# Performance work log

Measured on AMD Instinct MI355X. Metric: run time of the kernel, lower is better.

## Reference

```python
import jax, jax.numpy as jnp
import numpy as np

B, T, I, H, O = 64, 256, 128, 512, 64
GRAD_CLIP = 5.0


def setup_inputs() -> dict:
    key = jax.random.key(0)
    ks = jax.random.split(key, 20)
    sH = 1.0 / np.sqrt(H)
    sI = 1.0 / np.sqrt(I)
    f32 = jnp.float32
    return {
        "x": jax.random.normal(ks[0], (B, T, I), f32),
        "y": jax.random.randint(ks[1], (B,), 0, O),
        "W1w": jax.random.normal(ks[2], (H, H), f32) * sH,
        "V1w": jax.random.normal(ks[3], (H, I), f32) * sI,
        "V1b": jnp.zeros((H,), f32),
        "W2w": jax.random.normal(ks[4], (H, H), f32) * sH,
        "W2b": jnp.zeros((H,), f32),
        "V2w": jax.random.normal(ks[5], (H, I), f32) * sI,
        "W3w": jax.random.normal(ks[6], (H, H), f32) * sH,
        "W3b": jnp.zeros((H,), f32),
        "V3w": jax.random.normal(ks[7], (H, I), f32) * sI,
        "Woutw": jax.random.normal(ks[8], (O, H), f32) * sH,
        "Woutb": jnp.zeros((O,), f32),
        "BW1": jax.random.normal(ks[9], (O, H), f32) * sH,
        "BV1": jax.random.normal(ks[10], (O, H), f32) * sH,
        "BW2": jax.random.normal(ks[11], (O, H), f32) * sH,
        "BV2": jax.random.normal(ks[12], (O, H), f32) * sH,
        "BW3": jax.random.normal(ks[13], (O, H), f32) * sH,
        "BV3": jax.random.normal(ks[14], (O, H), f32) * sH,
    }


def reference(x, y, W1w, V1w, V1b, W2w, W2b, V2w, W3w, W3b, V3w,
              Woutw, Woutb, BW1, BV1, BW2, BV2, BW3, BV3):
    Bsz, Tlen, _ = x.shape
    Hd = W1w.shape[0]
    Od = Woutw.shape[0]
    h0 = jnp.zeros((Bsz, Hd), x.dtype)
    xt = jnp.swapaxes(x, 0, 1)  # [T, B, I]

    def step(h, xti):
        z = jax.nn.sigmoid(h @ W2w.T + W2b + xti @ V2w.T)
        r = jax.nn.sigmoid(h @ W3w.T + W3b + xti @ V3w.T)
        ht = jnp.tanh(xti @ V1w.T + V1b + (h * r) @ W1w.T)
        hn = (1.0 - z) * ht + z * h
        return hn, (r, z, ht, hn)

    hT, (rs, zs, hs, hid) = jax.lax.scan(step, h0, xt)  # each [T, B, H]
    output = jax.nn.softmax(hT @ Woutw.T + Woutb, axis=-1)
    error = output - jax.nn.one_hot(y, Od, dtype=output.dtype)

    BW1e, BV1e = error @ BW1, error @ BV1
    BW2e, BV2e = error @ BW2, error @ BV2
    BW3e, BV3e = error @ BW3, error @ BV3

    hiddens = jnp.concatenate([h0[None], hid], axis=0)  # [T+1, B, H]
    # Faithfully replicate torch's hiddens[t-1] list indexing: at t=0 this is
    # hiddens[-1], i.e. the FINAL hidden state (Python negative indexing).
    idx = (np.arange(Tlen) - 1) % (Tlen + 1)
    hprev = hiddens[idx]  # [T, B, H]

    rr = rs * (1.0 - rs)
    sz = 1.0 - zs
    dh = 1.0 - hs ** 2

    # z-gate terms (index 1) -- original code uses r*(1-r) here, replicated.
    zg = (hprev - hs) * rr
    zgV = zg * BV2e[None]
    zgW = zg * BW2e[None]
    dV1 = jnp.einsum('tbh,tbi->hi', zgV, xt) / Bsz
    dW1 = jnp.einsum('tbh,tbH->hH', zgW, hprev) / Bsz
    db1 = zgV.sum(0).mean(0)

    # r-gate terms (index 2)
    AV = ((BV3e[None] * sz * dh) @ W1w.T) * hprev * rr
    AW = ((BW3e[None] * sz * dh) @ W1w.T) * hprev * rr
    dV2 = jnp.einsum('tbh,tbi->hi', AV, xt) / Bsz
    dW2 = jnp.einsum('tbh,tbH->hH', AW, hprev) / Bsz
    db2 = AV.sum(0).mean(0)

    # h-gate terms (index 0)
    HV = ((BV1e[None] * sz) @ W1w.T) * dh
    HW = ((BW1e[None] * sz) @ W1w.T) * dh
    dV0 = jnp.einsum('tbh,tbi->hi', HV, xt) / Bsz
    dW0 = jnp.einsum('tbh,tbH->hH', HW, rs * hprev) / Bsz
    db0 = HV.sum(0).mean(0)

    def nc(g):
        g = g / jnp.linalg.norm(g)
        return jnp.clip(g, -GRAD_CLIP, GRAD_CLIP)

    return (output, hT,
            nc(dW0), nc(dW1), nc(dW2),
            nc(dV0), nc(dV1), nc(dV2),
            nc(db0), nc(db1), nc(db2),
            error)
```

## Files before the change

### kernel.cpp

```cpp
#include <hip/hip_runtime.h>
#include <hip/hip_bf16.h>

#define DI __device__ __forceinline__

typedef __bf16 bf16x8 __attribute__((ext_vector_type(8)));
typedef __bf16 bf16x4 __attribute__((ext_vector_type(4)));
typedef __bf16 bf16x2 __attribute__((ext_vector_type(2)));
typedef float  f32x4  __attribute__((ext_vector_type(4)));
typedef unsigned long long ull;

static constexpr int Bc = 64, Tc = 256, Ic = 128, Hc = 512, Oc = 64;
static constexpr int TBc = Tc * Bc;
static constexpr size_t THW = (size_t)TBc * Hc;

static constexpr size_t O_OUT = 0;
static constexpr size_t O_HT  = 4096;
static constexpr size_t O_DW0 = 36864;
static constexpr size_t O_DV0 = 823296;
static constexpr size_t O_DB0 = 1019904;
static constexpr size_t O_ERR = 1021440;

static constexpr size_t W_SLOT = 1024;
static constexpr size_t W_DB   = 2048;
static constexpr size_t W_FLG  = 8192;
static constexpr size_t W_ERRW = 16384;
static constexpr size_t W_PROJ = 32768;
static constexpr size_t W_W1B  = 819200;
static constexpr size_t W_HX   = 1343488;
static constexpr size_t W_HRX  = 1474560;
static constexpr size_t W_XT   = 1605632;
static constexpr size_t W_HIST = 5799936;
static constexpr size_t W_PB   = 72908800;
static constexpr size_t W_NEED = W_PB + 100663296;


DI void st32_agent(float* p, float v) {
  __hip_atomic_store((unsigned int*)p, __float_as_uint(v),
                     __ATOMIC_RELAXED, __HIP_MEMORY_SCOPE_AGENT);
}
DI ull ld64_agent(const void* p) {
  return __hip_atomic_load((ull*)p, __ATOMIC_RELAXED, __HIP_MEMORY_SCOPE_AGENT);
}

DI void group_barrier(int* flags_g, int myslot, int bar, bool& dead) {
  __syncthreads();
  if (threadIdx.x == 0)
    __hip_atomic_store(&flags_g[myslot * 32], bar,
                       __ATOMIC_RELAXED, __HIP_MEMORY_SCOPE_AGENT);
  if (threadIdx.x < 64 && !dead) {
    const int l = threadIdx.x;
    int spins = 0;
    for (;;) {
      int v = bar;
      if (l < 16)
        v = __hip_atomic_load(&flags_g[l * 32],
                              __ATOMIC_RELAXED, __HIP_MEMORY_SCOPE_AGENT);
      if (__all(v >= bar)) break;
      __builtin_amdgcn_s_sleep(1);
      if (++spins > 4000000) { dead = true; break; }
    }
  }
  __syncthreads();
}

DI float hprev_at(const __bf16* __restrict__ h_h, int k, int col) {
  int t = k >> 6;
  if (t == 1) return 0.f;
  int row = (t == 0) ? (16320 + (k & 63)) : (k - 128);
  return (float)h_h[(size_t)row * 512 + col];
}


__global__ void kzero(float* __restrict__ p, int n) {
  int i = blockIdx.x * 256 + threadIdx.x;
  if (i < n) p[i] = 0.f;
}
__global__ void ksent(float* p, float v) { p[0] = v; }
__global__ void k0_cast(const float* __restrict__ s, __bf16* __restrict__ d, int n) {
  int i = blockIdx.x * 256 + threadIdx.x;
  if (i < n) d[i] = (__bf16)s[i];
}

__global__ __launch_bounds__(256)
void k1_xv(const float* __restrict__ x, const float* __restrict__ V1w,
           const float* __restrict__ V2w, const float* __restrict__ V3w,
           const float* __restrict__ V1b, const float* __restrict__ W2b,
           const float* __restrict__ W3b,
           float* __restrict__ xv1f, float* __restrict__ xv2f, float* __restrict__ xv3f)
{
  const int cb = blockIdx.x, t = blockIdx.y;
  const int g = cb >> 3, jblk = cb & 7;
  const float* Vg   = (g == 0) ? V1w : (g == 1) ? V2w : V3w;
  const float* bias = (g == 0) ? V1b : (g == 1) ? W2b : W3b;
  float* of = (g == 0) ? xv1f : (g == 1) ? xv2f : xv3f;
  __shared__ float As[64 * 69];
  __shared__ float Bs[64 * 69];
  const int tid = threadIdx.x;
  float acc[4][4] = {};
  const int m0 = (tid & 15) * 4, j0 = (tid >> 4) * 4;
  for (int kc = 0; kc < 2; ++kc) {
    __syncthreads();
    #pragma unroll
    for (int e = 0; e < 4; ++e) {
      int idx = tid + e * 256;
      int row = idx >> 4, c4 = (idx & 15) * 4;
      float4 v = *reinterpret_cast<const float4*>(&x[((size_t)row * 256 + t) * 128 + kc * 64 + c4]);
      As[row * 69 + c4 + 0] = v.x; As[row * 69 + c4 + 1] = v.y;
      As[row * 69 + c4 + 2] = v.z; As[row * 69 + c4 + 3] = v.w;
      float4 w = *reinterpret_cast<const float4*>(&Vg[(size_t)(jblk * 64 + row) * 128 + kc * 64 + c4]);
      Bs[row * 69 + c4 + 0] = w.x; Bs[row * 69 + c4 + 1] = w.y;
      Bs[row * 69 + c4 + 2] = w.z; Bs[row * 69 + c4 + 3] = w.w;
    }
    __syncthreads();
    for (int i = 0; i < 64; ++i) {
      float a[4], b[4];
      #pragma unroll
      for (int u = 0; u < 4; ++u) a[u] = As[(m0 + u) * 69 + i];
      #pragma unroll
      for (int u = 0; u < 4; ++u) b[u] = Bs[(j0 + u) * 69 + i];
      #pragma unroll
      for (int mi = 0; mi < 4; ++mi)
        #pragma unroll
        for (int ji = 0; ji < 4; ++ji) acc[mi][ji] += a[mi] * b[ji];
    }
  }
  #pragma unroll
  for (int ji = 0; ji < 4; ++ji) {
    int jg = jblk * 64 + j0 + ji;
    float bv = bias[jg];
    #pragma unroll
    for (int mi = 0; mi < 4; ++mi) {
      int b = m0 + mi;
      of[((size_t)t * 64 + b) * 512 + jg] = acc[mi][ji] + bv;
    }
  }
}

__global__ void e0_xt(const float* __restrict__ x, __bf16* __restrict__ XT)
{
  const int t = blockIdx.x;
  __shared__ __bf16 xs[64 * 132];
  const int tid = threadIdx.x;
  #pragma unroll
  for (int e = 0; e < 8; ++e) {
    int idx = tid + e * 256;
    int b = idx >> 5, c4 = (idx & 31) * 4;
    float4 v = *reinterpret_cast<const float4*>(&x[((size_t)b * 256 + t) * 128 + c4]);
    xs[b * 132 + c4 + 0] = (__bf16)v.x; xs[b * 132 + c4 + 1] = (__bf16)v.y;
    xs[b * 132 + c4 + 2] = (__bf16)v.z; xs[b * 132 + c4 + 3] = (__bf16)v.w;
  }
  __syncthreads();
  #pragma unroll
  for (int e = 0; e < 8; ++e) {
    int idx = tid + e * 256;
    int i = idx >> 4, b4 = (idx & 15) * 4;
    __bf16* d = &XT[(size_t)i * TBc + t * 64 + b4];
    d[0] = xs[(b4 + 0) * 132 + i];
    d[1] = xs[(b4 + 1) * 132 + i];
    d[2] = xs[(b4 + 2) * 132 + i];
    d[3] = xs[(b4 + 3) * 132 + i];
  }
}

__global__ __launch_bounds__(256, 1)
void k2_recur(const float* __restrict__ W1w, const float* __restrict__ W2w,
              const float* __restrict__ W3w,
              const float* __restrict__ xv1, const float* __restrict__ xv2,
              const float* __restrict__ xv3,
              __bf16* __restrict__ r_h, __bf16* __restrict__ z_h,
              __bf16* __restrict__ ht_h, __bf16* __restrict__ h_h,
              float* __restrict__ hx, float* __restrict__ hrx,
              int* __restrict__ flags, float* __restrict__ dout)
{
  const int g  = blockIdx.x >> 4;
  const int cw = blockIdx.x & 15;
  const int tid = threadIdx.x, lane = tid & 63, wv = tid >> 6;
  const int kh = wv & 1;
  const int ct = wv >> 1;
  const int q  = lane >> 4;
  const int colc = cw * 32 + ct * 16 + (lane & 15);
  const bool owner = (kh == 0);

  __shared__ __align__(16) __bf16 c0[8192];
  __shared__ __align__(16) __bf16 c1[8192];
  __shared__ __align__(16) __bf16 c2[8192];
  __shared__ float pbuf[128 * 9];

  bf16x8 w1c[3][8], w2c[3][8], w3c[3][8];
  #pragma unroll
  for (int kk2 = 0; kk2 < 8; ++kk2) {
    const int kb = (kh * 8 + kk2) * 32 + q * 8;
    #pragma unroll
    for (int j = 0; j < 8; ++j) {
      float w = W1w[(size_t)colc * 512 + kb + j];
      __bf16 a = (__bf16)w; float r1 = w - (float)a;
      __bf16 b = (__bf16)r1;
      w1c[0][kk2][j] = a; w1c[1][kk2][j] = b; w1c[2][kk2][j] = (__bf16)(r1 - (float)b);
      w = W2w[(size_t)colc * 512 + kb + j];
      a = (__bf16)w; r1 = w - (float)a; b = (__bf16)r1;
      w2c[0][kk2][j] = a; w2c[1][kk2][j] = b; w2c[2][kk2][j] = (__bf16)(r1 - (float)b);
      w = W3w[(size_t)colc * 512 + kb + j];
      a = (__bf16)w; r1 = w - (float)a; b = (__bf16)r1;
      w3c[0][kk2][j] = a; w3c[1][kk2][j] = b; w3c[2][kk2][j] = (__bf16)(r1 - (float)b);
    }
  }
  for (int i = tid; i < 8192; i += 256) {
    c0[i] = (__bf16)0.f; c1[i] = (__bf16)0.f; c2[i] = (__bf16)0.f;
  }
  __syncthreads();

  float hreg[4] = {0.f, 0.f, 0.f, 0.f};
  float* hx_g  = hx  + g * 8192;
  float* hrx_g = hrx + g * 8192;
  int* flags_g = flags + g * 16 * 32;
  const int fragbase = (colc >> 5) * 512 + (((colc >> 3) & 3) * 16 + q * 4) * 8 + (colc & 7);
  const int pb = (ct * 64 + lane) * 9;

  auto stage = [&](const float* __restrict__ srcf) {
    const ull* src = reinterpret_cast<const ull*>(srcf);
    ull u[16];
    #pragma unroll
    for (int j = 0; j < 16; ++j) u[j] = ld64_agent(src + j * 256 + tid);
    #pragma unroll
    for (int j = 0; j < 16; ++j) {
      float f0 = __uint_as_float((unsigned int)u[j]);
      float f1 = __uint_as_float((unsigned int)(u[j] >> 32));
      __bf16 a0 = (__bf16)f0; float r0 = f0 - (float)a0; __bf16 b0 = (__bf16)r0;
      __bf16 d0 = (__bf16)(r0 - (float)b0);
      __bf16 a1 = (__bf16)f1; float r1 = f1 - (float)a1; __bf16 b1 = (__bf16)r1;
      __bf16 d1 = (__bf16)(r1 - (float)b1);
      int o = (j * 256 + tid) * 2;
      bf16x2 v0; v0[0] = a0; v0[1] = a1;
      bf16x2 v1; v1[0] = b0; v1[1] = b1;
      bf16x2 v2; v2[0] = d0; v2[1] = d1;
      *reinterpret_cast<bf16x2*>(&c0[o]) = v0;
      *reinterpret_cast<bf16x2*>(&c1[o]) = v1;
      *reinterpret_cast<bf16x2*>(&c2[o]) = v2;
    }
  };

  bool dead = false;
  int bar = 0;
  #pragma unroll 1
  for (int t = 0; t < Tc; ++t) {
    const size_t rowb = ((size_t)t * 64 + g * 16 + q * 4) * 512 + colc;
    float xv1v[4], xv2v[4], xv3v[4];
    if (owner) {
      #pragma unroll
      for (int i = 0; i < 4; ++i) {
        size_t o = rowb + (size_t)i * 512;
        xv1v[i] = xv1[o]; xv2v[i] = xv2[o]; xv3v[i] = xv3[o];
      }
    }
    f32x4 a2 = {0.f,0.f,0.f,0.f}, a3 = {0.f,0.f,0.f,0.f};
    #pragma unroll
    for (int kk2 = 0; kk2 < 8; ++kk2) {
      const int idx = (kh * 8 + kk2) * 512 + lane * 8;
      bf16x8 h0 = *reinterpret_cast<const bf16x8*>(&c0[idx]);
      bf16x8 h1 = *reinterpret_cast<const bf16x8*>(&c1[idx]);
      bf16x8 h2 = *reinterpret_cast<const bf16x8*>(&c2[idx]);
      a2 = __builtin_amdgcn_mfma_f32_16x16x32_bf16(h0, w2c[0][kk2], a2, 0, 0, 0);
      a2 = __builtin_amdgcn_mfma_f32_16x16x32_bf16(h1, w2c[0][kk2], a2, 0, 0, 0);
      a2 = __builtin_amdgcn_mfma_f32_16x16x32_bf16(h0, w2c[1][kk2], a2, 0, 0, 0);
      a2 = __builtin_amdgcn_mfma_f32_16x16x32_bf16(h2, w2c[0][kk2], a2, 0, 0, 0);
      a2 = __builtin_amdgcn_mfma_f32_16x16x32_bf16(h1, w2c[1][kk2], a2, 0, 0, 0);
      a2 = __builtin_amdgcn_mfma_f32_16x16x32_bf16(h0, w2c[2][kk2], a2, 0, 0, 0);
      a3 = __builtin_amdgcn_mfma_f32_16x16x32_bf16(h0, w3c[0][kk2], a3, 0, 0, 0);
      a3 = __builtin_amdgcn_mfma_f32_16x16x32_bf16(h1, w3c[0][kk2], a3, 0, 0, 0);
      a3 = __builtin_amdgcn_mfma_f32_16x16x32_bf16(h0, w3c[1][kk2], a3, 0, 0, 0);
      a3 = __builtin_amdgcn_mfma_f32_16x16x32_bf16(h2, w3c[0][kk2], a3, 0, 0, 0);
      a3 = __builtin_amdgcn_mfma_f32_16x16x32_bf16(h1, w3c[1][kk2], a3, 0, 0, 0);
      a3 = __builtin_amdgcn_mfma_f32_16x16x32_bf16(h0, w3c[2][kk2], a3, 0, 0, 0);
    }
    if (!owner) {
      #pragma unroll
      for (int i = 0; i < 4; ++i) { pbuf[pb + i] = a2[i]; pbuf[pb + 4 + i] = a3[i]; }
    }
    __syncthreads();
    float zz[4], rr4[4];
    if (owner) {
      #pragma unroll
      for (int i = 0; i < 4; ++i) {
        float s2 = a2[i] + pbuf[pb + i]     + xv2v[i];
        float s3 = a3[i] + pbuf[pb + 4 + i] + xv3v[i];
        zz[i]  = 1.f / (1.f + expf(-s2));
        rr4[i] = 1.f / (1.f + expf(-s3));
        st32_agent(&hrx_g[fragbase + i * 8], hreg[i] * rr4[i]);
      }
    }
    ++bar; group_barrier(flags_g, cw, bar, dead);
    if (owner) {
      #pragma unroll
      for (int i = 0; i < 4; ++i) {
        z_h[rowb + (size_t)i * 512] = (__bf16)zz[i];
        r_h[rowb + (size_t)i * 512] = (__bf16)rr4[i];
      }
    }
    stage(hrx_g);
    __syncthreads();
    f32x4 a1 = {0.f,0.f,0.f,0.f};
    #pragma unroll
    for (int kk2 = 0; kk2 < 8; ++kk2) {
      const int idx = (kh * 8 + kk2) * 512 + lane * 8;
      bf16x8 h0 = *reinterpret_cast<const bf16x8*>(&c0[idx]);
      bf16x8 h1 = *reinterpret_cast<const bf16x8*>(&c1[idx]);
      bf16x8 h2 = *reinterpret_cast<const bf16x8*>(&c2[idx]);
      a1 = __builtin_amdgcn_mfma_f32_16x16x32_bf16(h0, w1c[0][kk2], a1, 0, 0, 0);
      a1 = __builtin_amdgcn_mfma_f32_16x16x32_bf16(h1, w1c[0][kk2], a1, 0, 0, 0);
      a1 = __builtin_amdgcn_mfma_f32_16x16x32_bf16(h0, w1c[1][kk2], a1, 0, 0, 0);
      a1 = __builtin_amdgcn_mfma_f32_16x16x32_bf16(h2, w1c[0][kk2], a1, 0, 0, 0);
      a1 = __builtin_amdgcn_mfma_f32_16x16x32_bf16(h1, w1c[1][kk2], a1, 0, 0, 0);
      a1 = __builtin_amdgcn_mfma_f32_16x16x32_bf16(h0, w1c[2][kk2], a1, 0, 0, 0);
    }
    if (!owner) {
      #pragma unroll
      for (int i = 0; i < 4; ++i) pbuf[pb + i] = a1[i];
    }
    __syncthreads();
    float htv[4];
    if (owner) {
      #pragma unroll
      for (int i = 0; i < 4; ++i) {
        float pre = a1[i] + pbuf[pb + i] + xv1v[i];
        float ht = tanhf(pre);
        float hn = zz[i] * (hreg[i] - ht) + ht;
        htv[i] = ht;
        hreg[i] = hn;
        st32_agent(&hx_g[fragbase + i * 8], hn);
      }
    }
    ++bar; group_barrier(flags_g, cw, bar, dead);
    if (owner) {
      #pragma unroll
      for (int i = 0; i < 4; ++i) {
        ht_h[rowb + (size_t)i * 512] = (__bf16)htv[i];
        h_h[rowb + (size_t)i * 512]  = (__bf16)hreg[i];
      }
    }
    if (t + 1 < Tc) stage(hx_g);
    __syncthreads();
  }
  if (owner) {
    #pragma unroll
    for (int i = 0; i < 4; ++i) {
      int b = g * 16 + q * 4 + i;
      dout[O_HT + (size_t)b * 512 + colc] = hreg[i];
    }
  }
}

__global__ void k3a_soft(const float* __restrict__ Woutw, const float* __restrict__ Woutb,
                         const int* __restrict__ y, float* __restrict__ dout,
                         float* __restrict__ errw)
{
  const int b = blockIdx.x, o = threadIdx.x;
  const float* hrow = dout + O_HT + (size_t)b * 512;
  float sv = Woutb[o];
  for (int k = 0; k < 512; ++k) sv += hrow[k] * Woutw[(size_t)o * 512 + k];
  float mx = sv;
  for (int off = 32; off; off >>= 1) mx = fmaxf(mx, __shfl_xor(mx, off, 64));
  float e = expf(sv - mx);
  float sum = e;
  for (int off = 32; off; off >>= 1) sum += __shfl_xor(sum, off, 64);
  float outp = e / sum;
  float errv = outp - ((y[b] == o) ? 1.f : 0.f);
  dout[O_OUT + b * 64 + o] = outp;
  dout[O_ERR + b * 64 + o] = errv;
  errw[b * 64 + o] = errv;
}

__global__ __launch_bounds__(256)
void k3b_proj(const float* __restrict__ err,
              const float* b0, const float* b1, const float* b2,
              const float* b3, const float* b4, const float* b5,
              float* __restrict__ proj)
{
  const int p = blockIdx.y;
  const int hb = blockIdx.x * 64;
  const float* BX = (p==0)?b0:(p==1)?b1:(p==2)?b2:(p==3)?b3:(p==4)?b4:b5;
  __shared__ float es[64 * 64];
  __shared__ float bs[64 * 65];
  for (int i = threadIdx.x; i < 4096; i += 256) es[i] = err[i];
  for (int i = threadIdx.x; i < 4096; i += 256) {
    int o = i >> 6, hh = i & 63;
    bs[o * 65 + hh] = BX[(size_t)o * 512 + hb + hh];
  }
  __syncthreads();
  for (int e = 0; e < 16; ++e) {
    int idx = threadIdx.x + e * 256;
    int b = idx >> 6, hh = idx & 63;
    float s = 0.f;
    for (int o = 0; o < 64; ++o) s += es[b * 64 + o] * bs[o * 65 + hh];
    proj[(size_t)p * 32768 + b * 512 + hb + hh] = s;
  }
}

__global__ __launch_bounds__(256)
void e1t(const __bf16* __restrict__ r_h, const __bf16* __restrict__ h_h,
         __bf16* __restrict__ HpT, __bf16* __restrict__ RsHpT)
{
  const int t = blockIdx.y, hb = blockIdx.x * 64;
  const int tid = threadIdx.x;
  __shared__ __bf16 tr[64 * 68];
  float hpv[16], rv[16];
  #pragma unroll
  for (int e = 0; e < 16; ++e) {
    int idx = tid + e * 256;
    int b = idx >> 6, hl = idx & 63;
    hpv[e] = hprev_at(h_h, t * 64 + b, hb + hl);
    rv[e]  = (float)r_h[((size_t)t * 64 + b) * 512 + hb + hl];
  }
  for (int rnd = 0; rnd < 2; ++rnd) {
    __syncthreads();
    #pragma unroll
    for (int e = 0; e < 16; ++e) {
      int idx = tid + e * 256;
      int b = idx >> 6, hl = idx & 63;
      tr[b * 68 + hl] = (__bf16)(rnd == 0 ? hpv[e] : rv[e] * hpv[e]);
    }
    __syncthreads();
    __bf16* dst = (rnd == 0) ? HpT : RsHpT;
    #pragma unroll
    for (int e = 0; e < 16; ++e) {
      int idx = tid + e * 256;
      int hl2 = idx >> 6, b2 = idx & 63;
      dst[(size_t)(hb + hl2) * TBc + t * 64 + b2] = tr[b2 * 68 + hl2];
    }
  }
}

__global__ __launch_bounds__(256)
void k4_pgemm(const __bf16* __restrict__ z_h, const __bf16* __restrict__ ht_h,
              const __bf16* __restrict__ r_h, const __bf16* __restrict__ h_h,
              const float* __restrict__ proj, const __bf16* __restrict__ W1b,
              __bf16* __restrict__ P)
{
  const int p = blockIdx.z;
  const int krow0 = blockIdx.x * 128;
  const int n0 = blockIdx.y * 128;
  const int pidx = (p == 0) ? 5 : (p == 1) ? 4 : (p == 2) ? 1 : 0;
  const float* pr = proj + (size_t)pidx * 32768;
  const int tid = threadIdx.x, lane = tid & 63, wv = tid >> 6, q = lane >> 4;
  const int wm = (wv & 1) * 64, wn = (wv >> 1) * 64;
  __shared__ __align__(16) __bf16 Al[128 * 40];
  __shared__ __align__(16) __bf16 Bl[128 * 40];
  f32x4 acc[4][4] = {};
  for (int kt = 0; kt < 16; ++kt) {
    const int h0 = kt * 32;
    __syncthreads();
    #pragma unroll
    for (int e = 0; e < 4; ++e) {
      int idx = tid + e * 256;
      int row = idx >> 3, h4 = (idx & 7) * 4;
      int kg = krow0 + row;
      bf16x4 zz = *reinterpret_cast<const bf16x4*>(&z_h[(size_t)kg * 512 + h0 + h4]);
      bf16x4 tt = *reinterpret_cast<const bf16x4*>(&ht_h[(size_t)kg * 512 + h0 + h4]);
      float4 pv = *reinterpret_cast<const float4*>(&pr[(size_t)(kg & 63) * 512 + h0 + h4]);
      float pvv[4] = {pv.x, pv.y, pv.z, pv.w};
      bf16x4 gv;
      #pragma unroll
      for (int j = 0; j < 4; ++j) {
        float sz = 1.f - (float)zz[j];
        float v = pvv[j] * sz;
        if (p < 2) { float h = (float)tt[j]; v *= (1.f - h * h); }
        gv[j] = (__bf16)v;
      }
      *reinterpret_cast<bf16x4*>(&Al[row * 40 + h4]) = gv;
      bf16x4 wv4 = *reinterpret_cast<const bf16x4*>(&W1b[(size_t)(n0 + row) * 512 + h0 + h4]);
      *reinterpret_cast<bf16x4*>(&Bl[row * 40 + h4]) = wv4;
    }
    __syncthreads();
    bf16x8 af[4], bfv[4];
    #pragma unroll
    for (int mi = 0; mi < 4; ++mi)
      af[mi] = *reinterpret_cast<const bf16x8*>(&Al[(wm + mi * 16 + (lane & 15)) * 40 + q * 8]);
    #pragma unroll
    for (int ni = 0; ni < 4; ++ni)
      bfv[ni] = *reinterpret_cast<const bf16x8*>(&Bl[(wn + ni * 16 + (lane & 15)) * 40 + q * 8]);
    #pragma unroll
    for (int mi = 0; mi < 4; ++mi)
      #pragma unroll
      for (int ni = 0; ni < 4; ++ni)
        acc[mi][ni] = __builtin_amdgcn_mfma_f32_16x16x32_bf16(af[mi], bfv[ni], acc[mi][ni], 0, 0, 0);
  }
  __bf16* Pp = P + (size_t)p * THW;
  #pragma unroll
  for (int mi = 0; mi < 4; ++mi) {
    const int kg = krow0 + wm + mi * 16 + q * 4;
    const int tt = kg >> 6;
    #pragma unroll
    for (int ni = 0; ni < 4; ++ni) {
      const int n = n0 + wn + ni * 16 + (lane & 15);
      union { __bf16 b[4]; uint2 u; } pk;
      #pragma unroll
      for (int i = 0; i < 4; ++i) {
        float mul;
        if (p < 2) {
          float r = (float)r_h[(size_t)(kg + i) * 512 + n];
          float hp = 0.f;
          if (tt != 1) {
            int kr = (tt == 0) ? (16320 + (kg & 63) + i) : (kg + i - 128);
            hp = (float)h_h[(size_t)kr * 512 + n];
          }
          mul = hp * r * (1.f - r);
        } else {
          float h = (float)ht_h[(size_t)(kg + i) * 512 + n];
          mul = 1.f - h * h;
        }
        pk.b[i] = (__bf16)(acc[mi][ni][i] * mul);
      }
      *reinterpret_cast<uint2*>(&Pp[(size_t)n * TBc + kg]) = pk.u;
    }
  }
}

__global__ __launch_bounds__(256)
void k5_all(const __bf16* __restrict__ P, const __bf16* __restrict__ RsHpT,
            const __bf16* __restrict__ HpT, const __bf16* __restrict__ XT,
            const __bf16* __restrict__ r_h, const __bf16* __restrict__ ht_h,
            const __bf16* __restrict__ h_h, const float* __restrict__ proj,
            float* __restrict__ dout, float scale)
{
  const __bf16* Ap; int amode; const __bf16* Bp; const float* projA;
  float* out; int N; int m0i, n0i, zi;
  int b = blockIdx.x;
  if (b < 768) {
    int job = b >> 8, wb = b & 255;
    m0i = wb & 3; n0i = (wb >> 2) & 3; zi = wb >> 4;
    N = 512;
    out = dout + O_DW0 + (size_t)job * 262144;
    if (job == 0)      { Ap = P + 3 * THW; amode = 0; Bp = RsHpT; projA = proj; }
    else if (job == 1) { Ap = nullptr;     amode = 1; Bp = HpT;   projA = proj + 2 * 32768; }
    else               { Ap = P + 1 * THW; amode = 0; Bp = HpT;   projA = proj; }
  } else {
    int b2 = b - 768; int job = b2 >> 6, wb = b2 & 63;
    m0i = wb & 3; n0i = 0; zi = wb >> 2;
    N = 128;
    out = dout + O_DV0 + (size_t)job * 65536;
    if (job == 0)      { Ap = P + 2 * THW; amode = 0; Bp = XT; projA = proj; }
    else if (job == 1) { Ap = nullptr;     amode = 1; Bp = XT; projA = proj + 3 * 32768; }
    else               { Ap = P + 0 * THW; amode = 0; Bp = XT; projA = proj; }
  }
  const int m0 = m0i * 128;
  const int n0 = n0i * 128;
  const int klen = 1024;
  const int tid = threadIdx.x, lane = tid & 63, wv = tid >> 6, q = lane >> 4;
  const int wm = (wv & 1) * 64, wn = (wv >> 1) * 64;
  __shared__ __align__(16) __bf16 Al[128 * 72];
  __shared__ __align__(16) __bf16 Bl[128 * 72];
  f32x4 acc[4][4] = {};
  const int iters = klen >> 6;
  for (int kt = 0; kt < iters; ++kt) {
    const int kk0 = zi * klen + kt * 64;
    __syncthreads();
    #pragma unroll
    for (int e = 0; e < 8; ++e) {
      int idx = tid + e * 256;
      int row = idx >> 4, c4 = (idx & 15) * 4;
      bf16x4 bv = *reinterpret_cast<const bf16x4*>(&Bp[(size_t)(n0 + row) * TBc + kk0 + c4]);
      *reinterpret_cast<bf16x4*>(&Bl[row * 72 + c4]) = bv;
    }
    if (amode == 0) {
      #pragma unroll
      for (int e = 0; e < 8; ++e) {
        int idx = tid + e * 256;
        int row = idx >> 4, c4 = (idx & 15) * 4;
        bf16x4 av = *reinterpret_cast<const bf16x4*>(&Ap[(size_t)(m0 + row) * TBc + kk0 + c4]);
        *reinterpret_cast<bf16x4*>(&Al[row * 72 + c4]) = av;
      }
    } else {
      #pragma unroll
      for (int e = 0; e < 8; ++e) {
        int idx = tid + e * 256;
        int kk = idx >> 5;
        int m4 = (idx & 31) * 4;
        int kg = kk0 + kk;
        int tt = kg >> 6;
        bf16x4 hs = *reinterpret_cast<const bf16x4*>(&ht_h[(size_t)kg * 512 + m0 + m4]);
        bf16x4 rv = *reinterpret_cast<const bf16x4*>(&r_h[(size_t)kg * 512 + m0 + m4]);
        float4 pv = *reinterpret_cast<const float4*>(&projA[(size_t)(kg & 63) * 512 + m0 + m4]);
        float pvv[4] = {pv.x, pv.y, pv.z, pv.w};
        float hpf[4] = {0.f, 0.f, 0.f, 0.f};
        if (tt != 1) {
          int kr = (tt == 0) ? (16320 + (kg & 63)) : (kg - 128);
          bf16x4 hp = *reinterpret_cast<const bf16x4*>(&h_h[(size_t)kr * 512 + m0 + m4]);
          #pragma unroll
          for (int j = 0; j < 4; ++j) hpf[j] = (float)hp[j];
        }
        #pragma unroll
        for (int j = 0; j < 4; ++j) {
          float r = (float)rv[j];
          float zg = (hpf[j] - (float)hs[j]) * r * (1.f - r) * pvv[j];
          Al[(m4 + j) * 72 + kk] = (__bf16)zg;
        }
      }
    }
    __syncthreads();
    #pragma unroll
    for (int ks = 0; ks < 2; ++ks) {
      bf16x8 af[4], bfv[4];
      #pragma unroll
      for (int mi = 0; mi < 4; ++mi)
        af[mi] = *reinterpret_cast<const bf16x8*>(&Al[(wm + mi * 16 + (lane & 15)) * 72 + ks * 32 + q * 8]);
      #pragma unroll
      for (int ni = 0; ni < 4; ++ni)
        bfv[ni] = *reinterpret_cast<const bf16x8*>(&Bl[(wn + ni * 16 + (lane & 15)) * 72 + ks * 32 + q * 8]);
      #pragma unroll
      for (int mi = 0; mi < 4; ++mi)
        #pragma unroll
        for (int ni = 0; ni < 4; ++ni)
          acc[mi][ni] = __builtin_amdgcn_mfma_f32_16x16x32_bf16(af[mi], bfv[ni], acc[mi][ni], 0, 0, 0);
    }
  }
  #pragma unroll
  for (int mi = 0; mi < 4; ++mi) {
    const int m = m0 + wm + mi * 16 + q * 4;
    #pragma unroll
    for (int ni = 0; ni < 4; ++ni) {
      const int n = n0 + wn + ni * 16 + (lane & 15);
      #pragma unroll
      for (int i = 0; i < 4; ++i)
        atomicAdd(&out[(size_t)(m + i) * N + n], acc[mi][ni][i] * scale);
    }
  }
}

__global__ void k_dbP(const __bf16* __restrict__ P, float* __restrict__ db)
{
  const size_t plane = (blockIdx.y == 0) ? 2 : 0;
  const int dbo = (blockIdx.y == 0) ? 0 : 1024;
  const __bf16* row = P + plane * THW + (size_t)blockIdx.x * TBc;
  float sv = 0.f;
  for (int i = threadIdx.x; i < TBc; i += 256) sv += (float)row[i];
  for (int off = 32; off; off >>= 1) sv += __shfl_xor(sv, off, 64);
  __shared__ float red[4];
  if ((threadIdx.x & 63) == 0) red[threadIdx.x >> 6] = sv;
  __syncthreads();
  if (threadIdx.x == 0)
    atomicAdd(&db[dbo + blockIdx.x], (red[0] + red[1] + red[2] + red[3]) * (1.f / 64.f));
}

__global__ void k_dbzg(const __bf16* __restrict__ r_h, const __bf16* __restrict__ ht_h,
                       const __bf16* __restrict__ h_h, const float* __restrict__ proj,
                       float* __restrict__ db)
{
  const int hb = blockIdx.x * 64;
  const int col = hb + (threadIdx.x & 63);
  const int part = threadIdx.x >> 6;
  const int kb = blockIdx.y * 1024;
  float sum = 0.f;
  for (int k = kb + part; k < kb + 1024; k += 4) {
    float hs = (float)ht_h[(size_t)k * 512 + col];
    float r  = (float)r_h[(size_t)k * 512 + col];
    float hp = hprev_at(h_h, k, col);
    float pv = proj[3 * 32768 + (size_t)(k & 63) * 512 + col];
    sum += (hp - hs) * r * (1.f - r) * pv;
  }
  __shared__ float sred[4][64];
  sred[part][threadIdx.x & 63] = sum;
  __syncthreads();
  if (threadIdx.x < 64)
    atomicAdd(&db[512 + hb + threadIdx.x],
              (sred[0][threadIdx.x] + sred[1][threadIdx.x] +
               sred[2][threadIdx.x] + sred[3][threadIdx.x]) * (1.f / 64.f));
}

__global__ void k6a_sumsq(const float* __restrict__ dout, const float* __restrict__ db,
                          float* __restrict__ slots)
{
  const int yy = blockIdx.y;
  const float* src; int count;
  if (yy < 3)      { src = dout + O_DW0 + (size_t)yy * 262144; count = 262144; }
  else if (yy < 6) { src = dout + O_DV0 + (size_t)(yy - 3) * 65536; count = 65536; }
  else             { src = db + (size_t)(yy - 6) * 512; count = 512; }
  int start = blockIdx.x * 4096;
  if (start >= count) return;
  int end = min(start + 4096, count);
  float sp = 0.f;
  for (int i = start + threadIdx.x; i < end; i += 256) { float v = src[i]; sp += v * v; }
  for (int off = 32; off; off >>= 1) sp += __shfl_xor(sp, off, 64);
  __shared__ float red[4];
  if ((threadIdx.x & 63) == 0) red[threadIdx.x >> 6] = sp;
  __syncthreads();
  if (threadIdx.x == 0) atomicAdd(&slots[yy], red[0] + red[1] + red[2] + red[3]);
}

__global__ void k6b_write(const float* __restrict__ db,
                          const float* __restrict__ slots, float* __restrict__ dout)
{
  const int yy = blockIdx.y;
  const float* src; int count; size_t oo;
  if (yy < 3)      { oo = O_DW0 + (size_t)yy * 262144; src = dout + oo; count = 262144; }
  else if (yy < 6) { oo = O_DV0 + (size_t)(yy - 3) * 65536; src = dout + oo; count = 65536; }
  else             { oo = O_DB0 + (size_t)(yy - 6) * 512; src = db + (size_t)(yy - 6) * 512; count = 512; }
  int start = blockIdx.x * 4096;
  if (start >= count) return;
  int end = min(start + 4096, count);
  float inv = 1.f / sqrtf(slots[yy]);
  for (int i = start + threadIdx.x; i < end; i += 256) {
    float v = src[i] * inv;
    dout[oo + i] = fminf(fmaxf(v, -5.f), 5.f);
  }
}

extern "C" void kernel_launch(void* const* d_in, const int* in_sizes, int n_in,
                              void* d_out, int out_size, void* d_ws, size_t ws_size,
                              hipStream_t stream)
{
  const float* x     = (const float*)d_in[0];
  const int*   y     = (const int*)d_in[1];
  const float* W1w   = (const float*)d_in[2];
  const float* V1w   = (const float*)d_in[3];
  const float* V1b   = (const float*)d_in[4];
  const float* W2w   = (const float*)d_in[5];
  const float* W2b   = (const float*)d_in[6];
  const float* V2w   = (const float*)d_in[7];
  const float* W3w   = (const float*)d_in[8];
  const float* W3b   = (const float*)d_in[9];
  const float* V3w   = (const float*)d_in[10];
  const float* Woutw = (const float*)d_in[11];
  const float* Woutb = (const float*)d_in[12];
  const float* BW1   = (const float*)d_in[13];
  const float* BV1   = (const float*)d_in[14];
  const float* BW2   = (const float*)d_in[15];
  const float* BV2   = (const float*)d_in[16];
  const float* BW3   = (const float*)d_in[17];
  const float* BV3   = (const float*)d_in[18];
  float* dout = (float*)d_out;
  char* ws = (char*)d_ws;

  if (ws_size < W_NEED) { ksent<<<1, 1, 0, stream>>>(dout, (float)ws_size); return; }

  float*  slots = (float*)(ws + W_SLOT);
  float*  dbr   = (float*)(ws + W_DB);
  int*    flg   = (int*)(ws + W_FLG);
  float*  errw  = (float*)(ws + W_ERRW);
  float*  proj  = (float*)(ws + W_PROJ);
  __bf16* W1b   = (__bf16*)(ws + W_W1B);
  float*  hx    = (float*)(ws + W_HX);
  float*  hrx   = (float*)(ws + W_HRX);
  __bf16* XT    = (__bf16*)(ws + W_XT);
  __bf16* r_h   = (__bf16*)(ws + W_HIST);
  __bf16* z_h   = (__bf16*)(ws + W_HIST + 16777216);
  __bf16* ht_h  = (__bf16*)(ws + W_HIST + 33554432);
  __bf16* h_h   = (__bf16*)(ws + W_HIST + 50331648);
  char*   PB    = ws + W_PB;

  float* xv1 = (float*)PB;
  float* xv2 = (float*)(PB + 33554432);
  float* xv3 = (float*)(PB + 67108864);
  __bf16* P     = (__bf16*)PB;
  __bf16* HpT   = (__bf16*)(PB + 67108864);
  __bf16* RsHpT = (__bf16*)(PB + 83886080);

  kzero<<<16, 256, 0, stream>>>((float*)ws, 4096);
  kzero<<<3840, 256, 0, stream>>>(dout + O_DW0, 983040);
  k0_cast<<<1024, 256, 0, stream>>>(W1w, W1b, 262144);
  k1_xv<<<dim3(24, 256), 256, 0, stream>>>(x, V1w, V2w, V3w, V1b, W2b, W3b, xv1, xv2, xv3);
  e0_xt<<<256, 256, 0, stream>>>(x, XT);
  k2_recur<<<64, 256, 0, stream>>>(W1w, W2w, W3w, xv1, xv2, xv3,
                                   r_h, z_h, ht_h, h_h, hx, hrx, flg, dout);
  k3a_soft<<<64, 64, 0, stream>>>(Woutw, Woutb, y, dout, errw);
  k3b_proj<<<dim3(8, 6), 256, 0, stream>>>(errw, BW1, BV1, BW2, BV2, BW3, BV3, proj);
  e1t<<<dim3(8, 256), 256, 0, stream>>>(r_h, h_h, HpT, RsHpT);
  k_dbzg<<<dim3(8, 16), 256, 0, stream>>>(r_h, ht_h, h_h, proj, dbr);

  k4_pgemm<<<dim3(128, 4, 4), 256, 0, stream>>>(z_h, ht_h, r_h, h_h, proj, W1b, P);
  const float sc = 1.f / 64.f;
  k5_all<<<960, 256, 0, stream>>>(P, RsHpT, HpT, XT, r_h, ht_h, h_h, proj, dout, sc);
  k_dbP<<<dim3(512, 2), 256, 0, stream>>>(P, dbr);
  k6a_sumsq<<<dim3(64, 9), 256, 0, stream>>>(dout, dbr, slots);
  k6b_write<<<dim3(64, 9), 256, 0, stream>>>(dbr, slots, dout);
}
```

Before: 2.583 ms.

## Drop third bf16 split term in recurrence MFMAs and fold side kernels into recur

The recurrent matmuls previously emulated fp32 with a three-way bf16 split using six MFMAs per k-chunk. They now use a two-way split with three MFMAs, halving the matrix work and LDS staging on the serial critical path, at the cost of lower accuracy in h. Separately, the x transpose, W1 bf16 cast and gradient-buffer zeroing kernels are merged into the recurrence launch as extra blocks, so fewer launches are needed and that work overlaps the 64 recurrence blocks. Those extra blocks share the device with the spin-barrier group and could interfere with its scheduling.

```diff
diff --git a/kernel.cpp b/kernel.cpp
--- a/kernel.cpp
+++ b/kernel.cpp
@@ -76,10 +76,6 @@
   if (i < n) p[i] = 0.f;
 }
 __global__ void ksent(float* p, float v) { p[0] = v; }
-__global__ void k0_cast(const float* __restrict__ s, __bf16* __restrict__ d, int n) {
-  int i = blockIdx.x * 256 + threadIdx.x;
-  if (i < n) d[i] = (__bf16)s[i];
-}
 
 __global__ __launch_bounds__(256)
 void k1_xv(const float* __restrict__ x, const float* __restrict__ V1w,
@@ -136,32 +132,6 @@
   }
 }
 
-__global__ void e0_xt(const float* __restrict__ x, __bf16* __restrict__ XT)
-{
-  const int t = blockIdx.x;
-  __shared__ __bf16 xs[64 * 132];
-  const int tid = threadIdx.x;
-  #pragma unroll
-  for (int e = 0; e < 8; ++e) {
-    int idx = tid + e * 256;
-    int b = idx >> 5, c4 = (idx & 31) * 4;
-    float4 v = *reinterpret_cast<const float4*>(&x[((size_t)b * 256 + t) * 128 + c4]);
-    xs[b * 132 + c4 + 0] = (__bf16)v.x; xs[b * 132 + c4 + 1] = (__bf16)v.y;
-    xs[b * 132 + c4 + 2] = (__bf16)v.z; xs[b * 132 + c4 + 3] = (__bf16)v.w;
-  }
-  __syncthreads();
-  #pragma unroll
-  for (int e = 0; e < 8; ++e) {
-    int idx = tid + e * 256;
-    int i = idx >> 4, b4 = (idx & 15) * 4;
-    __bf16* d = &XT[(size_t)i * TBc + t * 64 + b4];
-    d[0] = xs[(b4 + 0) * 132 + i];
-    d[1] = xs[(b4 + 1) * 132 + i];
-    d[2] = xs[(b4 + 2) * 132 + i];
-    d[3] = xs[(b4 + 3) * 132 + i];
-  }
-}
-
 __global__ __launch_bounds__(256, 1)
 void k2_recur(const float* __restrict__ W1w, const float* __restrict__ W2w,
               const float* __restrict__ W3w,
@@ -170,42 +140,80 @@
               __bf16* __restrict__ r_h, __bf16* __restrict__ z_h,
               __bf16* __restrict__ ht_h, __bf16* __restrict__ h_h,
               float* __restrict__ hx, float* __restrict__ hrx,
-              int* __restrict__ flags, float* __restrict__ dout)
-{
-  const int g  = blockIdx.x >> 4;
-  const int cw = blockIdx.x & 15;
-  const int tid = threadIdx.x, lane = tid & 63, wv = tid >> 6;
+              int* __restrict__ flags, float* __restrict__ dout,
+              const float* __restrict__ x, __bf16* __restrict__ XT,
+              __bf16* __restrict__ W1b)
+{
+  __shared__ __align__(16) char smem[37376];
+  const int tid = threadIdx.x;
+  const int bid = blockIdx.x;
+
+  if (bid >= 64) {
+    if (bid < 320) {
+      const int t = bid - 64;
+      __bf16* xs = (__bf16*)smem;
+      #pragma unroll
+      for (int e = 0; e < 8; ++e) {
+        int idx = tid + e * 256;
+        int b = idx >> 5, c4 = (idx & 31) * 4;
+        float4 v = *reinterpret_cast<const float4*>(&x[((size_t)b * 256 + t) * 128 + c4]);
+        xs[b * 132 + c4 + 0] = (__bf16)v.x; xs[b * 132 + c4 + 1] = (__bf16)v.y;
+        xs[b * 132 + c4 + 2] = (__bf16)v.z; xs[b * 132 + c4 + 3] = (__bf16)v.w;
+      }
+      __syncthreads();
+      #pragma unroll
+      for (int e = 0; e < 8; ++e) {
+        int idx = tid + e * 256;
+        int i = idx >> 4, b4 = (idx & 15) * 4;
+        __bf16* d = &XT[(size_t)i * TBc + t * 64 + b4];
+        d[0] = xs[(b4 + 0) * 132 + i];
+        d[1] = xs[(b4 + 1) * 132 + i];
+        d[2] = xs[(b4 + 2) * 132 + i];
+        d[3] = xs[(b4 + 3) * 132 + i];
+      }
+    } else if (bid < 352) {
+      for (int i = (bid - 320) * 256 + tid; i < 262144; i += 32 * 256)
+        W1b[i] = (__bf16)W1w[i];
+    } else {
+      float* p = dout + O_DW0;
+      for (int i = (bid - 352) * 256 + tid; i < 983040; i += 64 * 256)
+        p[i] = 0.f;
+    }
+    return;
+  }
+
+  const int g  = bid >> 4;
+  const int cw = bid & 15;
+  const int lane = tid & 63, wv = tid >> 6;
   const int kh = wv & 1;
   const int ct = wv >> 1;
   const int q  = lane >> 4;
   const int colc = cw * 32 + ct * 16 + (lane & 15);
   const bool owner = (kh == 0);
 
-  __shared__ __align__(16) __bf16 c0[8192];
-  __shared__ __align__(16) __bf16 c1[8192];
-  __shared__ __align__(16) __bf16 c2[8192];
-  __shared__ float pbuf[128 * 9];
-
-  bf16x8 w1c[3][8], w2c[3][8], w3c[3][8];
+  __bf16* c0  = (__bf16*)smem;
+  __bf16* c1  = (__bf16*)(smem + 16384);
+  float*  pbuf = (float*)(smem + 32768);
+
+  bf16x8 w1c[2][8], w2c[2][8], w3c[2][8];
   #pragma unroll
   for (int kk2 = 0; kk2 < 8; ++kk2) {
     const int kb = (kh * 8 + kk2) * 32 + q * 8;
     #pragma unroll
     for (int j = 0; j < 8; ++j) {
       float w = W1w[(size_t)colc * 512 + kb + j];
-      __bf16 a = (__bf16)w; float r1 = w - (float)a;
-      __bf16 b = (__bf16)r1;
-      w1c[0][kk2][j] = a; w1c[1][kk2][j] = b; w1c[2][kk2][j] = (__bf16)(r1 - (float)b);
+      __bf16 a = (__bf16)w;
+      w1c[0][kk2][j] = a; w1c[1][kk2][j] = (__bf16)(w - (float)a);
       w = W2w[(size_t)colc * 512 + kb + j];
-      a = (__bf16)w; r1 = w - (float)a; b = (__bf16)r1;
-      w2c[0][kk2][j] = a; w2c[1][kk2][j] = b; w2c[2][kk2][j] = (__bf16)(r1 - (float)b);
+      a = (__bf16)w;
+      w2c[0][kk2][j] = a; w2c[1][kk2][j] = (__bf16)(w - (float)a);
       w = W3w[(size_t)colc * 512 + kb + j];
-      a = (__bf16)w; r1 = w - (float)a; b = (__bf16)r1;
-      w3c[0][kk2][j] = a; w3c[1][kk2][j] = b; w3c[2][kk2][j] = (__bf16)(r1 - (float)b);
+      a = (__bf16)w;
+      w3c[0][kk2][j] = a; w3c[1][kk2][j] = (__bf16)(w - (float)a);
     }
   }
   for (int i = tid; i < 8192; i += 256) {
-    c0[i] = (__bf16)0.f; c1[i] = (__bf16)0.f; c2[i] = (__bf16)0.f;
+    c0[i] = (__bf16)0.f; c1[i] = (__bf16)0.f;
   }
   __syncthreads();
 
@@ -225,17 +233,13 @@
     for (int j = 0; j < 16; ++j) {
       float f0 = __uint_as_float((unsigned int)u[j]);
       float f1 = __uint_as_float((unsigned int)(u[j] >> 32));
-      __bf16 a0 = (__bf16)f0; float r0 = f0 - (float)a0; __bf16 b0 = (__bf16)r0;
-      __bf16 d0 = (__bf16)(r0 - (float)b0);
-      __bf16 a1 = (__bf16)f1; float r1 = f1 - (float)a1; __bf16 b1 = (__bf16)r1;
-      __bf16 d1 = (__bf16)(r1 - (float)b1);
+      __bf16 a0 = (__bf16)f0; __bf16 b0 = (__bf16)(f0 - (float)a0);
+      __bf16 a1 = (__bf16)f1; __bf16 b1 = (__bf16)(f1 - (float)a1);
       int o = (j * 256 + tid) * 2;
       bf16x2 v0; v0[0] = a0; v0[1] = a1;
       bf16x2 v1; v1[0] = b0; v1[1] = b1;
-      bf16x2 v2; v2[0] = d0; v2[1] = d1;
       *reinterpret_cast<bf16x2*>(&c0[o]) = v0;
       *reinterpret_cast<bf16x2*>(&c1[o]) = v1;
-      *reinterpret_cast<bf16x2*>(&c2[o]) = v2;
     }
   };
 
@@ -258,19 +262,12 @@
       const int idx = (kh * 8 + kk2) * 512 + lane * 8;
       bf16x8 h0 = *reinterpret_cast<const bf16x8*>(&c0[idx]);
       bf16x8 h1 = *reinterpret_cast<const bf16x8*>(&c1[idx]);
-      bf16x8 h2 = *reinterpret_cast<const bf16x8*>(&c2[idx]);
       a2 = __builtin_amdgcn_mfma_f32_16x16x32_bf16(h0, w2c[0][kk2], a2, 0, 0, 0);
       a2 = __builtin_amdgcn_mfma_f32_16x16x32_bf16(h1, w2c[0][kk2], a2, 0, 0, 0);
       a2 = __builtin_amdgcn_mfma_f32_16x16x32_bf16(h0, w2c[1][kk2], a2, 0, 0, 0);
-      a2 = __builtin_amdgcn_mfma_f32_16x16x32_bf16(h2, w2c[0][kk2], a2, 0, 0, 0);
-      a2 = __builtin_amdgcn_mfma_f32_16x16x32_bf16(h1, w2c[1][kk2], a2, 0, 0, 0);
-      a2 = __builtin_amdgcn_mfma_f32_16x16x32_bf16(h0, w2c[2][kk2], a2, 0, 0, 0);
       a3 = __builtin_amdgcn_mfma_f32_16x16x32_bf16(h0, w3c[0][kk2], a3, 0, 0, 0);
       a3 = __builtin_amdgcn_mfma_f32_16x16x32_bf16(h1, w3c[0][kk2], a3, 0, 0, 0);
       a3 = __builtin_amdgcn_mfma_f32_16x16x32_bf16(h0, w3c[1][kk2], a3, 0, 0, 0);
-      a3 = __builtin_amdgcn_mfma_f32_16x16x32_bf16(h2, w3c[0][kk2], a3, 0, 0, 0);
-      a3 = __builtin_amdgcn_mfma_f32_16x16x32_bf16(h1, w3c[1][kk2], a3, 0, 0, 0);
-      a3 = __builtin_amdgcn_mfma_f32_16x16x32_bf16(h0, w3c[2][kk2], a3, 0, 0, 0);
     }
     if (!owner) {
       #pragma unroll
@@ -304,13 +301,9 @@
       const int idx = (kh * 8 + kk2) * 512 + lane * 8;
       bf16x8 h0 = *reinterpret_cast<const bf16x8*>(&c0[idx]);
       bf16x8 h1 = *reinterpret_cast<const bf16x8*>(&c1[idx]);
-      bf16x8 h2 = *reinterpret_cast<const bf16x8*>(&c2[idx]);
       a1 = __builtin_amdgcn_mfma_f32_16x16x32_bf16(h0, w1c[0][kk2], a1, 0, 0, 0);
       a1 = __builtin_amdgcn_mfma_f32_16x16x32_bf16(h1, w1c[0][kk2], a1, 0, 0, 0);
       a1 = __builtin_amdgcn_mfma_f32_16x16x32_bf16(h0, w1c[1][kk2], a1, 0, 0, 0);
-      a1 = __builtin_amdgcn_mfma_f32_16x16x32_bf16(h2, w1c[0][kk2], a1, 0, 0, 0);
-      a1 = __builtin_amdgcn_mfma_f32_16x16x32_bf16(h1, w1c[1][kk2], a1, 0, 0, 0);
-      a1 = __builtin_amdgcn_mfma_f32_16x16x32_bf16(h0, w1c[2][kk2], a1, 0, 0, 0);
     }
     if (!owner) {
       #pragma unroll
@@ -754,12 +747,10 @@
   __bf16* RsHpT = (__bf16*)(PB + 83886080);
 
   kzero<<<16, 256, 0, stream>>>((float*)ws, 4096);
-  kzero<<<3840, 256, 0, stream>>>(dout + O_DW0, 983040);
-  k0_cast<<<1024, 256, 0, stream>>>(W1w, W1b, 262144);
   k1_xv<<<dim3(24, 256), 256, 0, stream>>>(x, V1w, V2w, V3w, V1b, W2b, W3b, xv1, xv2, xv3);
-  e0_xt<<<256, 256, 0, stream>>>(x, XT);
-  k2_recur<<<64, 256, 0, stream>>>(W1w, W2w, W3w, xv1, xv2, xv3,
-                                   r_h, z_h, ht_h, h_h, hx, hrx, flg, dout);
+  k2_recur<<<416, 256, 0, stream>>>(W1w, W2w, W3w, xv1, xv2, xv3,
+                                    r_h, z_h, ht_h, h_h, hx, hrx, flg, dout,
+                                    x, XT, W1b);
   k3a_soft<<<64, 64, 0, stream>>>(Woutw, Woutb, y, dout, errw);
   k3b_proj<<<dim3(8, 6), 256, 0, stream>>>(errw, BW1, BV1, BW2, BV2, BW3, BV3, proj);
   e1t<<<dim3(8, 256), 256, 0, stream>>>(r_h, h_h, HpT, RsHpT);
```

After: 2.372 ms. 1.09x faster.
